# Kernel tuning notes

Measured on AMD Instinct MI355X. Metric: run time of the kernel, lower is better.

## Reference

```python
import jax, jax.numpy as jnp
import numpy as np

EPS = 1e-12  # torch F.normalize clamp

N, C, H, W = 32, 128, 128, 128
K = 64  # num_clusters


def setup_inputs() -> dict:
    key = jax.random.key(0)
    k1, k2, k3 = jax.random.split(key, 3)
    x = jax.random.normal(k1, (N, C, H, W), dtype=jnp.float32)
    conv_w = jax.random.normal(k2, (K, C), dtype=jnp.float32) * 0.1  # 1x1 conv weight, no bias
    centroids = jax.random.uniform(k3, (K, C), dtype=jnp.float32)   # torch.rand init
    return {"x": x, "conv_w": conv_w, "centroids": centroids}


def reference(x, conv_w, centroids):
    n, c = x.shape[:2]
    xf = x.reshape(n, c, -1)                       # [N, C, S], S = H*W
    # 1x1 conv == per-location matmul over channels
    soft_assign = jnp.einsum('kc,ncs->nks', conv_w, xf)
    soft_assign = jax.nn.softmax(soft_assign, axis=1)   # softmax over clusters
    # vlad[n,k,c] = sum_s a[n,k,s] * (x[n,c,s] - centroid[k,c])
    #            = (a @ x^T) - (sum_s a) * centroid   (avoids per-cluster residual tensors)
    vlad = jnp.einsum('nks,ncs->nkc', soft_assign, xf) \
           - soft_assign.sum(axis=-1)[..., None] * centroids[None, :, :]
    # intra-normalization over descriptor dim
    vlad = vlad / jnp.maximum(jnp.linalg.norm(vlad, axis=2, keepdims=True), EPS)
    flat = vlad.reshape(n, -1)                     # [N, K*C]
    flat = flat / jnp.maximum(jnp.linalg.norm(flat, axis=1, keepdims=True), EPS)
    return flat
```

## Files before the change

kernel.cpp:

```cpp
#include <hip/hip_runtime.h>
#include <hip/hip_bf16.h>

#define N_ 32
#define C_ 128
#define K_ 64
#define S_ 16384
#define TS 32
#define CHUNK 1024
#define NCHUNK (S_/CHUNK)
#define CP 136
#define LP 68
#define SP 40
#define EPS 1e-12f

typedef __attribute__((ext_vector_type(8))) short short8;
typedef __attribute__((ext_vector_type(4))) float floatx4;

__device__ inline unsigned short bfraw(float v) {
  return __builtin_bit_cast(unsigned short, __float2bfloat16(v));
}
__device__ inline float bff(unsigned short u) {
  union { unsigned int i; float f; } c; c.i = ((unsigned int)u) << 16; return c.f;
}

__global__ __launch_bounds__(256, 2) void vlad_main(
    const float* __restrict__ x, const float* __restrict__ w,
    float* __restrict__ vlad_acc, float* __restrict__ asum_g) {
  __shared__ unsigned short sXTh[TS * CP];
  __shared__ unsigned short sXTl[TS * CP];
  __shared__ float sLog[TS * LP];
  __shared__ unsigned short sPh[K_ * SP];
  __shared__ unsigned short sPl[K_ * SP];

  const int tid = threadIdx.x;
  const int lane = tid & 63;
  const int wv = tid >> 6;
  const int n = blockIdx.x >> 4;
  const int chunk = blockIdx.x & 15;
  const int sbase = chunk * CHUNK;

  const int lm = lane & 15;
  const int lq = lane >> 4;
  const int kb = lq * 8;

  short8 Wh[4], Wl[4];
  {
    const float* wp = w + (wv * 16 + lm) * C_;
#pragma unroll
    for (int ks = 0; ks < 4; ++ks) {
      const float* p = wp + ks * 32 + kb;
      float4 a = *(const float4*)p;
      float4 b = *(const float4*)(p + 4);
      float e[8] = {a.x, a.y, a.z, a.w, b.x, b.y, b.z, b.w};
#pragma unroll
      for (int j = 0; j < 8; ++j) {
        unsigned short h = bfraw(e[j]);
        Wh[ks][j] = (short)h;
        Wl[ks][j] = (short)bfraw(e[j] - bff(h));
      }
    }
  }

  floatx4 acc[2][4];
#pragma unroll
  for (int i = 0; i < 2; ++i)
#pragma unroll
    for (int j = 0; j < 4; ++j) acc[i][j] = (floatx4){0.f, 0.f, 0.f, 0.f};
  float accA[8];
#pragma unroll
  for (int i = 0; i < 8; ++i) accA[i] = 0.f;

  const int cA = tid & 127, hA = tid >> 7;
  const float* xstg = x + ((size_t)n * C_ + cA) * S_ + sbase + hA * 16;
  const int sC = tid >> 3, octC = tid & 7;

  for (int t = 0; t < CHUNK / TS; ++t) {
    const int s0 = sbase + t * TS;

    {
      const float* p = xstg + t * TS;
      float4 v0 = *(const float4*)(p + 0);
      float4 v1 = *(const float4*)(p + 4);
      float4 v2 = *(const float4*)(p + 8);
      float4 v3 = *(const float4*)(p + 12);
      float vv[16] = {v0.x,v0.y,v0.z,v0.w, v1.x,v1.y,v1.z,v1.w,
                      v2.x,v2.y,v2.z,v2.w, v3.x,v3.y,v3.z,v3.w};
      const int sb = hA * 16;
#pragma unroll
      for (int u = 0; u < 16; ++u) {
        unsigned short h = bfraw(vv[u]);
        sXTh[(sb + u) * CP + cA] = h;
        sXTl[(sb + u) * CP + cA] = bfraw(vv[u] - bff(h));
      }
    }
    __syncthreads();

#pragma unroll
    for (int st = 0; st < 2; ++st) {
      floatx4 D = {0.f, 0.f, 0.f, 0.f};
      const int srow = st * 16 + lm;
#pragma unroll
      for (int ks = 0; ks < 4; ++ks) {
        short8 Ah = *(const short8*)&sXTh[srow * CP + ks * 32 + kb];
        short8 Al = *(const short8*)&sXTl[srow * CP + ks * 32 + kb];
        D = __builtin_amdgcn_mfma_f32_16x16x32_bf16(Ah, Wh[ks], D, 0, 0, 0);
        D = __builtin_amdgcn_mfma_f32_16x16x32_bf16(Al, Wh[ks], D, 0, 0, 0);
        D = __builtin_amdgcn_mfma_f32_16x16x32_bf16(Ah, Wl[ks], D, 0, 0, 0);
      }
      const int sD = st * 16 + lq * 4;
      const int kcD = wv * 16 + lm;
#pragma unroll
      for (int r = 0; r < 4; ++r) sLog[(sD + r) * LP + kcD] = D[r];
    }
    __syncthreads();

    {
      float e[8];
      float m = -1e30f;
#pragma unroll
      for (int i = 0; i < 8; ++i) {
        e[i] = sLog[sC * LP + octC + 8 * i];
        m = fmaxf(m, e[i]);
      }
      m = fmaxf(m, __shfl_xor(m, 1));
      m = fmaxf(m, __shfl_xor(m, 2));
      m = fmaxf(m, __shfl_xor(m, 4));
      float sum = 0.f;
#pragma unroll
      for (int i = 0; i < 8; ++i) { e[i] = __expf(e[i] - m); sum += e[i]; }
      sum += __shfl_xor(sum, 1);
      sum += __shfl_xor(sum, 2);
      sum += __shfl_xor(sum, 4);
      float inv = 1.f / sum;
#pragma unroll
      for (int i = 0; i < 8; ++i) {
        float pr = e[i] * inv;
        accA[i] += pr;
        unsigned short h = bfraw(pr);
        sPh[(octC + 8 * i) * SP + sC] = h;
        sPl[(octC + 8 * i) * SP + sC] = bfraw(pr - bff(h));
      }
    }
    __syncthreads();

    {
      short8 Bh[4], Bl[4];
#pragma unroll
      for (int kt = 0; kt < 4; ++kt) {
        Bh[kt] = *(const short8*)&sPh[(kt * 16 + lm) * SP + kb];
        Bl[kt] = *(const short8*)&sPl[(kt * 16 + lm) * SP + kb];
      }
#pragma unroll
      for (int ci = 0; ci < 2; ++ci) {
        const int crow = (wv * 2 + ci) * 16 + lm;
        const float* xp = x + ((size_t)n * C_ + crow) * S_ + s0 + kb;
        float4 a = *(const float4*)xp;
        float4 b = *(const float4*)(xp + 4);
        float e[8] = {a.x, a.y, a.z, a.w, b.x, b.y, b.z, b.w};
        short8 Ah, Al;
#pragma unroll
        for (int j = 0; j < 8; ++j) {
          unsigned short h = bfraw(e[j]);
          Ah[j] = (short)h;
          Al[j] = (short)bfraw(e[j] - bff(h));
        }
#pragma unroll
        for (int kt = 0; kt < 4; ++kt) {
          acc[ci][kt] = __builtin_amdgcn_mfma_f32_16x16x32_bf16(Ah, Bh[kt], acc[ci][kt], 0, 0, 0);
          acc[ci][kt] = __builtin_amdgcn_mfma_f32_16x16x32_bf16(Al, Bh[kt], acc[ci][kt], 0, 0, 0);
          acc[ci][kt] = __builtin_amdgcn_mfma_f32_16x16x32_bf16(Ah, Bl[kt], acc[ci][kt], 0, 0, 0);
        }
      }
    }
    __syncthreads();
  }

  float* vb = vlad_acc + (size_t)n * K_ * C_;
#pragma unroll
  for (int ci = 0; ci < 2; ++ci) {
    const int c0 = (wv * 2 + ci) * 16 + lq * 4;
#pragma unroll
    for (int kt = 0; kt < 4; ++kt) {
      const int kc = kt * 16 + lm;
#pragma unroll
      for (int r = 0; r < 4; ++r)
        atomicAdd(vb + kc * C_ + c0 + r, acc[ci][kt][r]);
    }
  }

#pragma unroll
  for (int i = 0; i < 8; ++i) sLog[tid * 8 + i] = accA[i];
  __syncthreads();
  if (tid < K_) {
    float tsum = 0.f;
    for (int s8 = 0; s8 < 32; ++s8)
      tsum += sLog[(s8 * 8 + (tid & 7)) * 8 + (tid >> 3)];
    atomicAdd(asum_g + n * K_ + tid, tsum);
  }
}

__global__ __launch_bounds__(128) void vlad_intra(
    float* __restrict__ vlad_acc, const float* __restrict__ asum_g,
    const float* __restrict__ cent, float* __restrict__ gnorm) {
  const int bid = blockIdx.x;
  const int n = bid >> 6, k = bid & 63;
  const int c = threadIdx.x;
  const size_t base = ((size_t)(n * K_ + k)) * C_;
  float a = asum_g[n * K_ + k];
  float v = vlad_acc[base + c] - a * cent[k * C_ + c];
  float ss = v * v;
  ss += __shfl_xor(ss, 1);  ss += __shfl_xor(ss, 2);  ss += __shfl_xor(ss, 4);
  ss += __shfl_xor(ss, 8);  ss += __shfl_xor(ss, 16); ss += __shfl_xor(ss, 32);
  __shared__ float red[2];
  if ((threadIdx.x & 63) == 0) red[threadIdx.x >> 6] = ss;
  __syncthreads();
  float total = red[0] + red[1];
  float nrm = fmaxf(sqrtf(total), EPS);
  vlad_acc[base + c] = v / nrm;
  if (threadIdx.x == 0) atomicAdd(gnorm + n, total / (nrm * nrm));
}

__global__ __launch_bounds__(256) void vlad_final(
    const float* __restrict__ vlad_acc, const float* __restrict__ gnorm,
    float* __restrict__ out) {
  const int idx = blockIdx.x * 256 + threadIdx.x;
  if (idx >= N_ * K_ * C_) return;
  float g = gnorm[idx >> 13];
  out[idx] = vlad_acc[idx] / fmaxf(sqrtf(g), EPS);
}

extern "C" void kernel_launch(void* const* d_in, const int* in_sizes, int n_in,
                              void* d_out, int out_size, void* d_ws, size_t ws_size,
                              hipStream_t stream) {
  const float* x    = (const float*)d_in[0];
  const float* w    = (const float*)d_in[1];
  const float* cent = (const float*)d_in[2];
  float* out = (float*)d_out;

  float* vlad_acc = (float*)d_ws;
  float* asum_g   = vlad_acc + N_ * K_ * C_;
  float* gnorm    = asum_g + N_ * K_;

  const size_t zero_bytes = (size_t)(N_ * K_ * C_ + N_ * K_ + N_) * sizeof(float);
  hipMemsetAsync(d_ws, 0, zero_bytes, stream);

  vlad_main<<<dim3(N_ * NCHUNK), dim3(256), 0, stream>>>(x, w, vlad_acc, asum_g);
  vlad_intra<<<dim3(N_ * K_), dim3(128), 0, stream>>>(vlad_acc, asum_g, cent, gnorm);
  vlad_final<<<dim3((N_ * K_ * C_ + 255) / 256), dim3(256), 0, stream>>>(vlad_acc, gnorm, out);
}
```

Measured before the change: 496.1 us.

## Split more chunks, prefetch x, drop soft-assign low term, slab reduction

Doubles the chunk count to 32 per sample and raises the occupancy hint to 4 blocks per CU. It prefetches the next x tile into registers and hoists the second-GEMM x loads ahead of the softmax. The low-order bf16 term of the soft-assignment is dropped, cutting one third of the aggregation MFMAs and one LDS buffer at some cost in accuracy. When the workspace is large enough, per-block partial results are written to slabs and summed in the intra-normalization kernel instead of using atomics.

```diff
diff --git a/kernel.cpp b/kernel.cpp
--- a/kernel.cpp
+++ b/kernel.cpp
@@ -6,8 +6,9 @@
 #define K_ 64
 #define S_ 16384
 #define TS 32
-#define CHUNK 1024
-#define NCHUNK (S_/CHUNK)
+#define NCHUNK 32
+#define CHUNK (S_/NCHUNK)
+#define NITER (CHUNK/TS)
 #define CP 136
 #define LP 68
 #define SP 40
@@ -23,20 +24,20 @@
   union { unsigned int i; float f; } c; c.i = ((unsigned int)u) << 16; return c.f;
 }
 
-__global__ __launch_bounds__(256, 2) void vlad_main(
+template <bool SLAB>
+__global__ __launch_bounds__(256, 4) void vlad_main(
     const float* __restrict__ x, const float* __restrict__ w,
-    float* __restrict__ vlad_acc, float* __restrict__ asum_g) {
+    float* __restrict__ vlad_out, float* __restrict__ asum_out) {
   __shared__ unsigned short sXTh[TS * CP];
   __shared__ unsigned short sXTl[TS * CP];
   __shared__ float sLog[TS * LP];
   __shared__ unsigned short sPh[K_ * SP];
-  __shared__ unsigned short sPl[K_ * SP];
 
   const int tid = threadIdx.x;
   const int lane = tid & 63;
   const int wv = tid >> 6;
-  const int n = blockIdx.x >> 4;
-  const int chunk = blockIdx.x & 15;
+  const int n = blockIdx.x >> 5;
+  const int chunk = blockIdx.x & 31;
   const int sbase = chunk * CHUNK;
 
   const int lm = lane & 15;
@@ -74,17 +75,17 @@
   const float* xstg = x + ((size_t)n * C_ + cA) * S_ + sbase + hA * 16;
   const int sC = tid >> 3, octC = tid & 7;
 
-  for (int t = 0; t < CHUNK / TS; ++t) {
+  float4 p0 = *(const float4*)(xstg + 0);
+  float4 p1 = *(const float4*)(xstg + 4);
+  float4 p2 = *(const float4*)(xstg + 8);
+  float4 p3 = *(const float4*)(xstg + 12);
+
+  for (int t = 0; t < NITER; ++t) {
     const int s0 = sbase + t * TS;
 
     {
-      const float* p = xstg + t * TS;
-      float4 v0 = *(const float4*)(p + 0);
-      float4 v1 = *(const float4*)(p + 4);
-      float4 v2 = *(const float4*)(p + 8);
-      float4 v3 = *(const float4*)(p + 12);
-      float vv[16] = {v0.x,v0.y,v0.z,v0.w, v1.x,v1.y,v1.z,v1.w,
-                      v2.x,v2.y,v2.z,v2.w, v3.x,v3.y,v3.z,v3.w};
+      float vv[16] = {p0.x,p0.y,p0.z,p0.w, p1.x,p1.y,p1.z,p1.w,
+                      p2.x,p2.y,p2.z,p2.w, p3.x,p3.y,p3.z,p3.w};
       const int sb = hA * 16;
 #pragma unroll
       for (int u = 0; u < 16; ++u) {
@@ -92,6 +93,13 @@
         sXTh[(sb + u) * CP + cA] = h;
         sXTl[(sb + u) * CP + cA] = bfraw(vv[u] - bff(h));
       }
+    }
+    if (t + 1 < NITER) {
+      const float* p = xstg + (t + 1) * TS;
+      p0 = *(const float4*)(p + 0);
+      p1 = *(const float4*)(p + 4);
+      p2 = *(const float4*)(p + 8);
+      p3 = *(const float4*)(p + 12);
     }
     __syncthreads();
 
@@ -114,7 +122,17 @@
     }
     __syncthreads();
 
+    short8 Ah2[2], Al2[2];
     {
+      float4 xa[2], xb[2];
+#pragma unroll
+      for (int ci = 0; ci < 2; ++ci) {
+        const int crow = (wv * 2 + ci) * 16 + lm;
+        const float* xp = x + ((size_t)n * C_ + crow) * S_ + s0 + kb;
+        xa[ci] = *(const float4*)xp;
+        xb[ci] = *(const float4*)(xp + 4);
+      }
+
       float e[8];
       float m = -1e30f;
 #pragma unroll
@@ -136,55 +154,54 @@
       for (int i = 0; i < 8; ++i) {
         float pr = e[i] * inv;
         accA[i] += pr;
-        unsigned short h = bfraw(pr);
-        sPh[(octC + 8 * i) * SP + sC] = h;
-        sPl[(octC + 8 * i) * SP + sC] = bfraw(pr - bff(h));
+        sPh[(octC + 8 * i) * SP + sC] = bfraw(pr);
+      }
+
+#pragma unroll
+      for (int ci = 0; ci < 2; ++ci) {
+        float ee[8] = {xa[ci].x, xa[ci].y, xa[ci].z, xa[ci].w,
+                       xb[ci].x, xb[ci].y, xb[ci].z, xb[ci].w};
+#pragma unroll
+        for (int j = 0; j < 8; ++j) {
+          unsigned short h = bfraw(ee[j]);
+          Ah2[ci][j] = (short)h;
+          Al2[ci][j] = (short)bfraw(ee[j] - bff(h));
+        }
       }
     }
     __syncthreads();
 
     {
-      short8 Bh[4], Bl[4];
-#pragma unroll
-      for (int kt = 0; kt < 4; ++kt) {
+      short8 Bh[4];
+#pragma unroll
+      for (int kt = 0; kt < 4; ++kt)
         Bh[kt] = *(const short8*)&sPh[(kt * 16 + lm) * SP + kb];
-        Bl[kt] = *(const short8*)&sPl[(kt * 16 + lm) * SP + kb];
-      }
 #pragma unroll
       for (int ci = 0; ci < 2; ++ci) {
-        const int crow = (wv * 2 + ci) * 16 + lm;
-        const float* xp = x + ((size_t)n * C_ + crow) * S_ + s0 + kb;
-        float4 a = *(const float4*)xp;
-        float4 b = *(const float4*)(xp + 4);
-        float e[8] = {a.x, a.y, a.z, a.w, b.x, b.y, b.z, b.w};
-        short8 Ah, Al;
-#pragma unroll
-        for (int j = 0; j < 8; ++j) {
-          unsigned short h = bfraw(e[j]);
-          Ah[j] = (short)h;
-          Al[j] = (short)bfraw(e[j] - bff(h));
+#pragma unroll
+        for (int kt = 0; kt < 4; ++kt) {
+          acc[ci][kt] = __builtin_amdgcn_mfma_f32_16x16x32_bf16(Ah2[ci], Bh[kt], acc[ci][kt], 0, 0, 0);
+          acc[ci][kt] = __builtin_amdgcn_mfma_f32_16x16x32_bf16(Al2[ci], Bh[kt], acc[ci][kt], 0, 0, 0);
         }
-#pragma unroll
-        for (int kt = 0; kt < 4; ++kt) {
-          acc[ci][kt] = __builtin_amdgcn_mfma_f32_16x16x32_bf16(Ah, Bh[kt], acc[ci][kt], 0, 0, 0);
-          acc[ci][kt] = __builtin_amdgcn_mfma_f32_16x16x32_bf16(Al, Bh[kt], acc[ci][kt], 0, 0, 0);
-          acc[ci][kt] = __builtin_amdgcn_mfma_f32_16x16x32_bf16(Ah, Bl[kt], acc[ci][kt], 0, 0, 0);
-        }
-      }
-    }
-    __syncthreads();
-  }
-
-  float* vb = vlad_acc + (size_t)n * K_ * C_;
+      }
+    }
+    __syncthreads();
+  }
+
+  float* vb = vlad_out + (SLAB ? (size_t)blockIdx.x : (size_t)n) * (K_ * C_);
 #pragma unroll
   for (int ci = 0; ci < 2; ++ci) {
     const int c0 = (wv * 2 + ci) * 16 + lq * 4;
 #pragma unroll
     for (int kt = 0; kt < 4; ++kt) {
       const int kc = kt * 16 + lm;
-#pragma unroll
-      for (int r = 0; r < 4; ++r)
-        atomicAdd(vb + kc * C_ + c0 + r, acc[ci][kt][r]);
+      if (SLAB) {
+        *(floatx4*)(vb + kc * C_ + c0) = acc[ci][kt];
+      } else {
+#pragma unroll
+        for (int r = 0; r < 4; ++r)
+          atomicAdd(vb + kc * C_ + c0 + r, acc[ci][kt][r]);
+      }
     }
   }
 
@@ -195,19 +212,34 @@
     float tsum = 0.f;
     for (int s8 = 0; s8 < 32; ++s8)
       tsum += sLog[(s8 * 8 + (tid & 7)) * 8 + (tid >> 3)];
-    atomicAdd(asum_g + n * K_ + tid, tsum);
-  }
-}
-
+    if (SLAB) asum_out[(size_t)blockIdx.x * K_ + tid] = tsum;
+    else atomicAdd(asum_out + n * K_ + tid, tsum);
+  }
+}
+
+template <bool SLAB>
 __global__ __launch_bounds__(128) void vlad_intra(
-    float* __restrict__ vlad_acc, const float* __restrict__ asum_g,
-    const float* __restrict__ cent, float* __restrict__ gnorm) {
+    const float* __restrict__ vlad_in, const float* __restrict__ asum_in,
+    const float* __restrict__ cent, float* __restrict__ vlad_norm,
+    float* __restrict__ gnorm) {
   const int bid = blockIdx.x;
   const int n = bid >> 6, k = bid & 63;
   const int c = threadIdx.x;
-  const size_t base = ((size_t)(n * K_ + k)) * C_;
-  float a = asum_g[n * K_ + k];
-  float v = vlad_acc[base + c] - a * cent[k * C_ + c];
+
+  float v, a;
+  if (SLAB) {
+    v = 0.f; a = 0.f;
+#pragma unroll 4
+    for (int ch = 0; ch < NCHUNK; ++ch) {
+      v += vlad_in[((size_t)(n * NCHUNK + ch) * K_ + k) * C_ + c];
+      a += asum_in[(n * NCHUNK + ch) * K_ + k];
+    }
+  } else {
+    v = vlad_in[((size_t)(n * K_ + k)) * C_ + c];
+    a = asum_in[n * K_ + k];
+  }
+  v -= a * cent[k * C_ + c];
+
   float ss = v * v;
   ss += __shfl_xor(ss, 1);  ss += __shfl_xor(ss, 2);  ss += __shfl_xor(ss, 4);
   ss += __shfl_xor(ss, 8);  ss += __shfl_xor(ss, 16); ss += __shfl_xor(ss, 32);
@@ -216,17 +248,17 @@
   __syncthreads();
   float total = red[0] + red[1];
   float nrm = fmaxf(sqrtf(total), EPS);
-  vlad_acc[base + c] = v / nrm;
+  vlad_norm[((size_t)(n * K_ + k)) * C_ + c] = v / nrm;
   if (threadIdx.x == 0) atomicAdd(gnorm + n, total / (nrm * nrm));
 }
 
 __global__ __launch_bounds__(256) void vlad_final(
-    const float* __restrict__ vlad_acc, const float* __restrict__ gnorm,
+    const float* __restrict__ vlad_norm, const float* __restrict__ gnorm,
     float* __restrict__ out) {
   const int idx = blockIdx.x * 256 + threadIdx.x;
   if (idx >= N_ * K_ * C_) return;
   float g = gnorm[idx >> 13];
-  out[idx] = vlad_acc[idx] / fmaxf(sqrtf(g), EPS);
+  out[idx] = vlad_norm[idx] / fmaxf(sqrtf(g), EPS);
 }
 
 extern "C" void kernel_launch(void* const* d_in, const int* in_sizes, int n_in,
@@ -237,14 +269,28 @@
   const float* cent = (const float*)d_in[2];
   float* out = (float*)d_out;
 
-  float* vlad_acc = (float*)d_ws;
-  float* asum_g   = vlad_acc + N_ * K_ * C_;
-  float* gnorm    = asum_g + N_ * K_;
-
-  const size_t zero_bytes = (size_t)(N_ * K_ * C_ + N_ * K_ + N_) * sizeof(float);
-  hipMemsetAsync(d_ws, 0, zero_bytes, stream);
-
-  vlad_main<<<dim3(N_ * NCHUNK), dim3(256), 0, stream>>>(x, w, vlad_acc, asum_g);
-  vlad_intra<<<dim3(N_ * K_), dim3(128), 0, stream>>>(vlad_acc, asum_g, cent, gnorm);
-  vlad_final<<<dim3((N_ * K_ * C_ + 255) / 256), dim3(256), 0, stream>>>(vlad_acc, gnorm, out);
-}
+  const int nblk = N_ * NCHUNK;
+  const size_t slab_f  = (size_t)nblk * K_ * C_;
+  const size_t asum_f  = (size_t)nblk * K_;
+  const size_t norm_f  = (size_t)N_ * K_ * C_;
+  const size_t need = (slab_f + asum_f + norm_f + N_) * sizeof(float);
+
+  if (ws_size >= need) {
+    float* slab   = (float*)d_ws;
+    float* asums  = slab + slab_f;
+    float* vnorm  = asums + asum_f;
+    float* gnorm  = vnorm + norm_f;
+    hipMemsetAsync(gnorm, 0, N_ * sizeof(float), stream);
+    vlad_main<true><<<dim3(nblk), dim3(256), 0, stream>>>(x, w, slab, asums);
+    vlad_intra<true><<<dim3(N_ * K_), dim3(128), 0, stream>>>(slab, asums, cent, vnorm, gnorm);
+    vlad_final<<<dim3((N_ * K_ * C_ + 255) / 256), dim3(256), 0, stream>>>(vnorm, gnorm, out);
+  } else {
+    float* vlad_acc = (float*)d_ws;
+    float* asum_g   = vlad_acc + norm_f;
+    float* gnorm    = asum_g + N_ * K_;
+    hipMemsetAsync(d_ws, 0, (norm_f + N_ * K_ + N_) * sizeof(float), stream);
+    vlad_main<false><<<dim3(nblk), dim3(256), 0, stream>>>(x, w, vlad_acc, asum_g);
+    vlad_intra<false><<<dim3(N_ * K_), dim3(128), 0, stream>>>(vlad_acc, asum_g, cent, vlad_acc, gnorm);
+    vlad_final<<<dim3((N_ * K_ * C_ + 255) / 256), dim3(256), 0, stream>>>(vlad_acc, gnorm, out);
+  }
+}
```

New measurement: 442.6 us. 1.12x faster.
